# Performance work log

Hardware: AMD Instinct MI355X
Metric: run time of the kernel (lower is better)

## Reference

```python
import jax, jax.numpy as jnp
import numpy as np

D = 1024
H = 16
HD = D // H  # 64


def setup_inputs() -> dict:
    key = jax.random.key(0)
    ks = jax.random.split(key, 11)
    B, L = 2, 2048
    std = 0.02
    return {
        "query": jax.random.normal(ks[0], (B, L, D), jnp.float32),
        "key": jax.random.normal(ks[1], (B, L, D), jnp.float32),
        "value": jax.random.normal(ks[2], (B, L, D), jnp.float32),
        "Wq": jax.random.normal(ks[3], (D, D), jnp.float32) * std,
        "bq": jnp.zeros((D,), jnp.float32),
        "Wk": jax.random.normal(ks[4], (D, D), jnp.float32) * std,
        "bk": jnp.zeros((D,), jnp.float32),
        "Wv": jax.random.normal(ks[5], (D, D), jnp.float32) * std,
        "bv": jnp.zeros((D,), jnp.float32),
        "Wo": jax.random.normal(ks[6], (D, D), jnp.float32) * std,
        "bo": jnp.zeros((D,), jnp.float32),
    }


def _split_heads(x):
    # [B, L, D] -> [B, H, L, HD]
    B, L, _ = x.shape
    return x.reshape(B, L, H, HD).transpose(0, 2, 1, 3)


def reference(query, key, value, Wq, bq, Wk, bk, Wv, bv, Wo, bo):
    B, Lq, _ = query.shape
    # Linear projections (torch Linear: x @ W.T + b)
    Q = _split_heads(query @ Wq.T + bq)
    K = _split_heads(key @ Wk.T + bk)
    V = _split_heads(value @ Wv.T + bv)
    scale = HD ** -0.5
    scores = jnp.einsum("bhqd,bhkd->bhqk", Q, K) * scale  # [B,H,Lq,Lk]
    weights = jax.nn.softmax(scores, axis=-1)
    attended = jnp.einsum("bhqk,bhkd->bhqd", weights, V)  # [B,H,Lq,HD]
    attended = attended.transpose(0, 2, 1, 3).reshape(B, Lq, D)
    output = attended @ Wo.T + bo
    return output, weights.mean(axis=1)
```

## Files before the change

### kernel.cpp

```cpp
#include <hip/hip_runtime.h>
#include <stdint.h>

#define D_MODEL 1024
#define NHEAD 16
#define HDIM 64
#define SEQ 2048
#define NTOK 4096
#define KVB 128
#define NT (KVB / 16)

typedef unsigned short u16;
typedef float f32x4 __attribute__((ext_vector_type(4)));
typedef __bf16 bf16x8 __attribute__((ext_vector_type(8)));
typedef unsigned int u32x4 __attribute__((ext_vector_type(4)));
typedef u16 u16x4 __attribute__((ext_vector_type(4)));

#define QSC 0.180336880111117f

__device__ __forceinline__ u16 fcast_bf(float f) {
  __bf16 h = (__bf16)f;
  return __builtin_bit_cast(u16, h);
}

__device__ __forceinline__ float exp2_fast(float x) {
#if __has_builtin(__builtin_amdgcn_exp2f)
  return __builtin_amdgcn_exp2f(x);
#else
  return __expf(x * 0.69314718056f);
#endif
}

__device__ __forceinline__ bf16x8 scale_q(bf16x8 q) {
  bf16x8 r;
#pragma unroll
  for (int i = 0; i < 8; i++) r[i] = (__bf16)((float)q[i] * QSC);
  return r;
}

__device__ __forceinline__ bf16x8 lds_frag(const u16* sm, int off) {
  return *reinterpret_cast<const bf16x8*>(sm + off);
}

__device__ __forceinline__ void gload_lds16(const u16* g, u16* l) {
  __builtin_amdgcn_global_load_lds((const __attribute__((address_space(1))) void*)g,
                                   (__attribute__((address_space(3))) void*)l, 16, 0, 0);
}

__global__ void cvt3_kernel(const float* __restrict__ s0, const float* __restrict__ s1,
                            const float* __restrict__ s2, u16* __restrict__ dst, int n4) {
  const float* s = blockIdx.y == 0 ? s0 : (blockIdx.y == 1 ? s1 : s2);
  u16* d = dst + (size_t)blockIdx.y * n4 * 4;
  int i = blockIdx.x * blockDim.x + threadIdx.x;
  int stride = gridDim.x * blockDim.x;
  for (; i < n4; i += stride) {
    f32x4 v = reinterpret_cast<const f32x4*>(s)[i];
    u16x4 o;
    o[0] = fcast_bf(v[0]); o[1] = fcast_bf(v[1]);
    o[2] = fcast_bf(v[2]); o[3] = fcast_bf(v[3]);
    reinterpret_cast<u16x4*>(d)[i] = o;
  }
}

__global__ void cvt4_kernel(const float* __restrict__ s0, const float* __restrict__ s1,
                            const float* __restrict__ s2, const float* __restrict__ s3,
                            u16* __restrict__ dst, int n4) {
  const float* s = blockIdx.y == 0 ? s0 : (blockIdx.y == 1 ? s1 : (blockIdx.y == 2 ? s2 : s3));
  u16* d = dst + (size_t)blockIdx.y * n4 * 4;
  int i = blockIdx.x * blockDim.x + threadIdx.x;
  int stride = gridDim.x * blockDim.x;
  for (; i < n4; i += stride) {
    f32x4 v = reinterpret_cast<const f32x4*>(s)[i];
    u16x4 o;
    o[0] = fcast_bf(v[0]); o[1] = fcast_bf(v[1]);
    o[2] = fcast_bf(v[2]); o[3] = fcast_bf(v[3]);
    reinterpret_cast<u16x4*>(d)[i] = o;
  }
}

template<int MODE>
__global__ __launch_bounds__(256)
void gemm_kernel(const u16* __restrict__ Abase, const u16* __restrict__ Wbase,
                 const float* __restrict__ b0, const float* __restrict__ b1,
                 const float* __restrict__ b2,
                 u16* __restrict__ obf, float* __restrict__ of32) {
  const int z = (MODE == 0) ? blockIdx.z : 0;
  const u16* A = Abase + (size_t)z * NTOK * D_MODEL;
  const u16* W = Wbase + (size_t)z * D_MODEL * D_MODEL;
  const float* bias = (MODE == 0) ? (z == 0 ? b0 : (z == 1 ? b1 : b2)) : b0;
  u16* oz = (MODE == 0) ? (obf + (size_t)z * NTOK * D_MODEL) : obf;

  const int flat = blockIdx.y * 8 + blockIdx.x;
  const int nf = (flat & 7) * 32 + (flat >> 3);
  const int bn0 = (nf & 7) * 128;
  const int bm0 = (nf >> 3) * 128;
  const int tid = threadIdx.x;
  const int lane = tid & 63, wid = tid >> 6;
  const int wm = wid >> 1, wn = wid & 1;
  const int l15 = lane & 15, l4 = lane >> 4;
  const int lrow8 = lane >> 3, lch = lane & 7;

  __shared__ u16 smA[128 * 64];
  __shared__ u16 smB[128 * 64];

  f32x4 acc[4][4];
#pragma unroll
  for (int mi = 0; mi < 4; mi++)
#pragma unroll
    for (int ni = 0; ni < 4; ni++) acc[mi][ni] = f32x4{0.f, 0.f, 0.f, 0.f};

  for (int it = 0; it < D_MODEL / 64; it++) {
    const int k0 = it * 64;
    __syncthreads();
#pragma unroll
    for (int c2 = 0; c2 < 4; c2++) {
      int blk = wid * 4 + c2;
      int base16 = blk * 512;
      int row = blk * 8 + lrow8;
      gload_lds16(A + (size_t)(bm0 + row) * D_MODEL + k0 + lch * 8, &smA[base16]);
      gload_lds16(W + (size_t)(bn0 + row) * D_MODEL + k0 + lch * 8, &smB[base16]);
    }
    __syncthreads();
#pragma unroll
    for (int kk = 0; kk < 2; kk++) {
      bf16x8 af[4], bfv[4];
#pragma unroll
      for (int mi = 0; mi < 4; mi++) {
        int r = wm * 64 + mi * 16 + l15;
        af[mi] = lds_frag(smA, r * 64 + (kk * 4 + l4) * 8);
      }
#pragma unroll
      for (int ni = 0; ni < 4; ni++) {
        int r = wn * 64 + ni * 16 + l15;
        bfv[ni] = lds_frag(smB, r * 64 + (kk * 4 + l4) * 8);
      }
#pragma unroll
      for (int mi = 0; mi < 4; mi++)
#pragma unroll
        for (int ni = 0; ni < 4; ni++)
          acc[mi][ni] = __builtin_amdgcn_mfma_f32_16x16x32_bf16(af[mi], bfv[ni], acc[mi][ni], 0, 0, 0);
    }
  }

#pragma unroll
  for (int mi = 0; mi < 4; mi++) {
#pragma unroll
    for (int ni = 0; ni < 4; ni++) {
      int colg = bn0 + wn * 64 + ni * 16 + l15;
      float bv = bias[colg];
      if (MODE == 0 && z == 2) {
        int h = colg >> 6, hd = colg & 63;
        int row0 = bm0 + wm * 64 + mi * 16 + l4 * 4;
        int b = row0 >> 11, lq = row0 & 2047;
        u16x4 pk;
#pragma unroll
        for (int j = 0; j < 4; j++) pk[j] = fcast_bf(acc[mi][ni][j] + bv);
        size_t idx = ((size_t)((b * NHEAD + h) * HDIM + hd)) * SEQ + lq;
        *reinterpret_cast<u16x4*>(oz + idx) = pk;
      } else {
#pragma unroll
        for (int j = 0; j < 4; j++) {
          int rowg = bm0 + wm * 64 + mi * 16 + l4 * 4 + j;
          float v = acc[mi][ni][j] + bv;
          if (MODE == 0) {
            int b = rowg >> 11, lq = rowg & 2047;
            int h = colg >> 6, hd = colg & 63;
            oz[((size_t)((b * NHEAD + h) * SEQ + lq)) * HDIM + hd] = fcast_bf(v);
          } else {
            of32[(size_t)rowg * D_MODEL + colg] = v;
          }
        }
      }
    }
  }
}

__global__ __launch_bounds__(512)
void attn_kernel(const u16* __restrict__ Qh, const u16* __restrict__ Kh,
                 const u16* __restrict__ Vh, u16* __restrict__ attb,
                 float* __restrict__ m_ws, float* __restrict__ linv_ws) {
  const int qt0 = blockIdx.x * 128;
  const int bh = blockIdx.y;
  const int b = bh >> 4, h = bh & 15;
  const int tid = threadIdx.x;
  const int lane = tid & 63, wid = tid >> 6;
  const int l15 = lane & 15, l4 = lane >> 4;

  const u16* Qp = Qh + (size_t)bh * SEQ * HDIM;
  const u16* Kp = Kh + (size_t)bh * SEQ * HDIM;
  const u16* Vp = Vh + (size_t)bh * HDIM * SEQ;

  __shared__ u16 smK[KVB * 64];
  __shared__ u16 smV[64 * KVB];
  __shared__ u16 smP[8][16 * KVB];

  bf16x8 qf[2];
  {
    const u16* qrow = Qp + (size_t)(qt0 + wid * 16 + l15) * HDIM;
    qf[0] = scale_q(*reinterpret_cast<const bf16x8*>(qrow + l4 * 8));
    qf[1] = scale_q(*reinterpret_cast<const bf16x8*>(qrow + 32 + l4 * 8));
  }

  float m = -1e30f, lsum = 0.f;
  f32x4 oacc[4];
#pragma unroll
  for (int d = 0; d < 4; d++) oacc[d] = f32x4{0.f, 0.f, 0.f, 0.f};

  u32x4 rk[2], rv[2];
#pragma unroll
  for (int i = 0; i < 2; i++) {
    int c = i * 512 + tid;
    rk[i] = *reinterpret_cast<const u32x4*>(Kp + (size_t)(c >> 3) * HDIM + (c & 7) * 8);
    rv[i] = *reinterpret_cast<const u32x4*>(Vp + (size_t)(c >> 4) * SEQ + (c & 15) * 8);
  }

  for (int kt = 0; kt < SEQ / KVB; kt++) {
    __syncthreads();
#pragma unroll
    for (int i = 0; i < 2; i++) {
      int c = i * 512 + tid;
      { int row = c >> 3, ch = c & 7;
        *reinterpret_cast<u32x4*>(&smK[row * 64 + ((ch ^ (row & 7)) * 8)]) = rk[i]; }
      { int row = c >> 4, ch = c & 15;
        *reinterpret_cast<u32x4*>(&smV[row * KVB + ((ch ^ (row & 15)) * 8)]) = rv[i]; }
    }
    __syncthreads();
    if (kt + 1 < SEQ / KVB) {
      int kn = (kt + 1) * KVB;
#pragma unroll
      for (int i = 0; i < 2; i++) {
        int c = i * 512 + tid;
        rk[i] = *reinterpret_cast<const u32x4*>(Kp + (size_t)(kn + (c >> 3)) * HDIM + (c & 7) * 8);
        rv[i] = *reinterpret_cast<const u32x4*>(Vp + (size_t)(c >> 4) * SEQ + kn + (c & 15) * 8);
      }
    }
    f32x4 s[NT];
#pragma unroll
    for (int nt = 0; nt < NT; nt++) s[nt] = f32x4{0.f, 0.f, 0.f, 0.f};
#pragma unroll
    for (int kk = 0; kk < 2; kk++) {
#pragma unroll
      for (int nt = 0; nt < NT; nt++) {
        int r = nt * 16 + l15;
        int ch = (kk * 4 + l4) ^ (r & 7);
        bf16x8 kf = lds_frag(smK, r * 64 + ch * 8);
        s[nt] = __builtin_amdgcn_mfma_f32_16x16x32_bf16(kf, qf[kk], s[nt], 0, 0, 0);
      }
    }
    float smax = s[0][0];
#pragma unroll
    for (int nt = 0; nt < NT; nt++)
#pragma unroll
      for (int j = 0; j < 4; j++) smax = fmaxf(smax, s[nt][j]);
    smax = fmaxf(smax, __shfl_xor(smax, 16));
    smax = fmaxf(smax, __shfl_xor(smax, 32));
    float mn = fmaxf(m, smax);
    float corr = exp2_fast(m - mn);
    m = mn;
    float ps = 0.f;
#pragma unroll
    for (int nt = 0; nt < NT; nt++) {
      u16x4 pwv;
#pragma unroll
      for (int j = 0; j < 4; j++) {
        float pv = exp2_fast(s[nt][j] - mn);
        ps += pv;
        pwv[j] = fcast_bf(pv);
      }
      int sp = (nt * 4 + l4) ^ (l15 * 2);
      *reinterpret_cast<u16x4*>(&smP[wid][l15 * KVB + sp * 4]) = pwv;
    }
    ps += __shfl_xor(ps, 16);
    ps += __shfl_xor(ps, 32);
    lsum = lsum * corr + ps;
#pragma unroll
    for (int d = 0; d < 4; d++)
#pragma unroll
      for (int j = 0; j < 4; j++) oacc[d][j] *= corr;
#pragma unroll
    for (int kc = 0; kc < 4; kc++) {
      int chp = (kc * 4 + l4) ^ l15;
      bf16x8 pf = lds_frag(smP[wid], l15 * KVB + chp * 8);
#pragma unroll
      for (int d = 0; d < 4; d++) {
        int r = d * 16 + l15;
        int ch = (kc * 4 + l4) ^ (r & 15);
        bf16x8 vf = lds_frag(smV, r * KVB + ch * 8);
        oacc[d] = __builtin_amdgcn_mfma_f32_16x16x32_bf16(vf, pf, oacc[d], 0, 0, 0);
      }
    }
  }

  const float li = 1.f / lsum;
  const int token = qt0 + wid * 16 + l15;
  if (l4 == 0) {
    m_ws[(size_t)bh * SEQ + token] = m;
    linv_ws[(size_t)bh * SEQ + token] = li;
  }
#pragma unroll
  for (int d = 0; d < 4; d++) {
    u16x4 pk;
#pragma unroll
    for (int j = 0; j < 4; j++) pk[j] = fcast_bf(oacc[d][j] * li);
    *reinterpret_cast<u16x4*>(
        attb + ((size_t)(b * SEQ + token)) * D_MODEL + h * HDIM + d * 16 + l4 * 4) = pk;
  }
}

__global__ __launch_bounds__(512)
void mean_kernel(const u16* __restrict__ Qh, const u16* __restrict__ Kh,
                 const float* __restrict__ m_ws, const float* __restrict__ linv_ws,
                 float* __restrict__ out1) {
  const int kt0 = blockIdx.x * 128;
  const int qt0 = blockIdx.y * 128;
  const int b = blockIdx.z;
  const int tid = threadIdx.x;
  const int lane = tid & 63, wid = tid >> 6;
  const int l15 = lane & 15, l4 = lane >> 4;

  __shared__ u16 smK[2][2][64 * 64];

  f32x4 macc[2][4];
#pragma unroll
  for (int t = 0; t < 2; t++)
#pragma unroll
    for (int nt = 0; nt < 4; nt++) macc[t][nt] = f32x4{0.f, 0.f, 0.f, 0.f};

  const int rbase = qt0 + wid * 16 + l4 * 4;
  const size_t qoff = (size_t)(qt0 + wid * 16 + l15) * HDIM;
  const int srow = tid >> 3, sch = tid & 7;
  const int soff = srow * 64 + ((sch ^ (srow & 7)) * 8);

  u32x4 rk[2];
  bf16x8 qfa, qfb;
  {
    const u16* Kp0 = Kh + (size_t)(b * NHEAD) * SEQ * HDIM;
#pragma unroll
    for (int t = 0; t < 2; t++)
      rk[t] = *reinterpret_cast<const u32x4*>(Kp0 + (size_t)(kt0 + t * 64 + srow) * HDIM + sch * 8);
    const u16* Qp0 = Qh + (size_t)(b * NHEAD) * SEQ * HDIM + qoff;
    qfa = scale_q(*reinterpret_cast<const bf16x8*>(Qp0 + l4 * 8));
    qfb = scale_q(*reinterpret_cast<const bf16x8*>(Qp0 + 32 + l4 * 8));
  }

  for (int h = 0; h < NHEAD; h++) {
    const int bh = b * NHEAD + h;
#pragma unroll
    for (int t = 0; t < 2; t++)
      *reinterpret_cast<u32x4*>(&smK[h & 1][t][soff]) = rk[t];
    __syncthreads();
    u32x4 rkn[2];
    bf16x8 qfan, qfbn;
    if (h + 1 < NHEAD) {
      const u16* Kp1 = Kh + (size_t)(bh + 1) * SEQ * HDIM;
#pragma unroll
      for (int t = 0; t < 2; t++)
        rkn[t] = *reinterpret_cast<const u32x4*>(Kp1 + (size_t)(kt0 + t * 64 + srow) * HDIM + sch * 8);
      const u16* Qp1 = Qh + (size_t)(bh + 1) * SEQ * HDIM + qoff;
      qfan = scale_q(*reinterpret_cast<const bf16x8*>(Qp1 + l4 * 8));
      qfbn = scale_q(*reinterpret_cast<const bf16x8*>(Qp1 + 32 + l4 * 8));
    }
    f32x4 mv = *reinterpret_cast<const f32x4*>(&m_ws[(size_t)bh * SEQ + rbase]);
    f32x4 lv = *reinterpret_cast<const f32x4*>(&linv_ws[(size_t)bh * SEQ + rbase]);
#pragma unroll
    for (int t = 0; t < 2; t++) {
      const u16* kbuf = &smK[h & 1][t][0];
      f32x4 s[4];
#pragma unroll
      for (int nt = 0; nt < 4; nt++) s[nt] = f32x4{0.f, 0.f, 0.f, 0.f};
#pragma unroll
      for (int kk = 0; kk < 2; kk++) {
#pragma unroll
        for (int nt = 0; nt < 4; nt++) {
          int r = nt * 16 + l15;
          int ch = (kk * 4 + l4) ^ (r & 7);
          bf16x8 kf = lds_frag(kbuf, r * 64 + ch * 8);
          s[nt] = __builtin_amdgcn_mfma_f32_16x16x32_bf16(kk == 0 ? qfa : qfb, kf, s[nt], 0, 0, 0);
        }
      }
#pragma unroll
      for (int nt = 0; nt < 4; nt++)
#pragma unroll
        for (int j = 0; j < 4; j++)
          macc[t][nt][j] += exp2_fast(s[nt][j] - mv[j]) * lv[j];
    }
    if (h + 1 < NHEAD) {
      rk[0] = rkn[0]; rk[1] = rkn[1];
      qfa = qfan; qfb = qfbn;
    }
  }
  const float invh = 1.f / 16.f;
#pragma unroll
  for (int t = 0; t < 2; t++)
#pragma unroll
    for (int nt = 0; nt < 4; nt++)
#pragma unroll
      for (int j = 0; j < 4; j++)
        out1[((size_t)(b * SEQ + rbase + j)) * SEQ + kt0 + t * 64 + nt * 16 + l15] =
            macc[t][nt][j] * invh;
}

extern "C" void kernel_launch(void* const* d_in, const int* in_sizes, int n_in,
                              void* d_out, int out_size, void* d_ws, size_t ws_size,
                              hipStream_t stream) {
  (void)in_sizes; (void)n_in; (void)out_size; (void)ws_size;
  const float* query = (const float*)d_in[0];
  const float* key = (const float*)d_in[1];
  const float* value = (const float*)d_in[2];
  const float* Wq = (const float*)d_in[3];
  const float* bq = (const float*)d_in[4];
  const float* Wk = (const float*)d_in[5];
  const float* bk = (const float*)d_in[6];
  const float* Wv = (const float*)d_in[7];
  const float* bv = (const float*)d_in[8];
  const float* Wo = (const float*)d_in[9];
  const float* bo = (const float*)d_in[10];

  char* ws = (char*)d_ws;
  u16* xb = (u16*)(ws);
  u16* wb = (u16*)(ws + 25165824);
  u16* Qhp = (u16*)(ws + 33554432);
  u16* attb = (u16*)(ws + 58720256);
  float* m_ws = (float*)(ws + 67108864);
  float* linv_ws = (float*)(ws + 67371008);

  float* out0 = (float*)d_out;
  float* out1 = out0 + (size_t)NTOK * D_MODEL;

  cvt3_kernel<<<dim3(512, 3), 256, 0, stream>>>(query, key, value, xb, 1048576);
  cvt4_kernel<<<dim3(192, 4), 256, 0, stream>>>(Wq, Wk, Wv, Wo, wb, 262144);

  gemm_kernel<0><<<dim3(8, 32, 3), 256, 0, stream>>>(xb, wb, bq, bk, bv, Qhp, nullptr);
  attn_kernel<<<dim3(16, 32), 512, 0, stream>>>(Qhp, Qhp + 4194304, Qhp + 8388608,
                                                attb, m_ws, linv_ws);
  mean_kernel<<<dim3(16, 16, 2), 512, 0, stream>>>(Qhp, Qhp + 4194304, m_ws, linv_ws, out1);
  gemm_kernel<1><<<dim3(8, 32, 1), 256, 0, stream>>>(attb, wb + 3 * 1048576, bo, bo, bo,
                                                     nullptr, out0);
}
```

Measured before the change: 190.3 us.

## Merge conversion launches and co-schedule weight-mean with output projection

The two fp32-to-bf16 conversion kernels become one launch over seven sources. The separate mean-weights kernel and output-projection GEMM become one 768-block 'tail' launch, with blocks split by index between the two jobs. This removes launch gaps and lets the bandwidth-bound mean work overlap the MFMA-bound projection. The projection part uses 512 threads with a 2x4 per-wave tile, so each wave computes half as many outputs and has less reuse per LDS load than the old 256-thread kernel.

```diff
diff --git a/kernel.cpp b/kernel.cpp
--- a/kernel.cpp
+++ b/kernel.cpp
@@ -46,48 +46,36 @@
                                    (__attribute__((address_space(3))) void*)l, 16, 0, 0);
 }
 
-__global__ void cvt3_kernel(const float* __restrict__ s0, const float* __restrict__ s1,
-                            const float* __restrict__ s2, u16* __restrict__ dst, int n4) {
-  const float* s = blockIdx.y == 0 ? s0 : (blockIdx.y == 1 ? s1 : s2);
-  u16* d = dst + (size_t)blockIdx.y * n4 * 4;
+__global__ void cvt_all_kernel(const float* __restrict__ q, const float* __restrict__ k,
+                               const float* __restrict__ v, const float* __restrict__ wq,
+                               const float* __restrict__ wk, const float* __restrict__ wv,
+                               const float* __restrict__ wo, u16* __restrict__ dst) {
+  const int y = blockIdx.y;
+  const float* s = y == 0 ? q : (y == 1 ? k : (y == 2 ? v : (y == 3 ? wq :
+                   (y == 4 ? wk : (y == 5 ? wv : wo)))));
+  const int n4 = y < 3 ? 1048576 : 262144;
+  const size_t off4 = y < 3 ? (size_t)y * 1048576 : 3145728 + (size_t)(y - 3) * 262144;
+  u16x4* d = reinterpret_cast<u16x4*>(dst) + off4;
   int i = blockIdx.x * blockDim.x + threadIdx.x;
   int stride = gridDim.x * blockDim.x;
   for (; i < n4; i += stride) {
-    f32x4 v = reinterpret_cast<const f32x4*>(s)[i];
+    f32x4 vv = reinterpret_cast<const f32x4*>(s)[i];
     u16x4 o;
-    o[0] = fcast_bf(v[0]); o[1] = fcast_bf(v[1]);
-    o[2] = fcast_bf(v[2]); o[3] = fcast_bf(v[3]);
-    reinterpret_cast<u16x4*>(d)[i] = o;
-  }
-}
-
-__global__ void cvt4_kernel(const float* __restrict__ s0, const float* __restrict__ s1,
-                            const float* __restrict__ s2, const float* __restrict__ s3,
-                            u16* __restrict__ dst, int n4) {
-  const float* s = blockIdx.y == 0 ? s0 : (blockIdx.y == 1 ? s1 : (blockIdx.y == 2 ? s2 : s3));
-  u16* d = dst + (size_t)blockIdx.y * n4 * 4;
-  int i = blockIdx.x * blockDim.x + threadIdx.x;
-  int stride = gridDim.x * blockDim.x;
-  for (; i < n4; i += stride) {
-    f32x4 v = reinterpret_cast<const f32x4*>(s)[i];
-    u16x4 o;
-    o[0] = fcast_bf(v[0]); o[1] = fcast_bf(v[1]);
-    o[2] = fcast_bf(v[2]); o[3] = fcast_bf(v[3]);
-    reinterpret_cast<u16x4*>(d)[i] = o;
-  }
-}
-
-template<int MODE>
+    o[0] = fcast_bf(vv[0]); o[1] = fcast_bf(vv[1]);
+    o[2] = fcast_bf(vv[2]); o[3] = fcast_bf(vv[3]);
+    d[i] = o;
+  }
+}
+
 __global__ __launch_bounds__(256)
-void gemm_kernel(const u16* __restrict__ Abase, const u16* __restrict__ Wbase,
-                 const float* __restrict__ b0, const float* __restrict__ b1,
-                 const float* __restrict__ b2,
-                 u16* __restrict__ obf, float* __restrict__ of32) {
-  const int z = (MODE == 0) ? blockIdx.z : 0;
+void gemm_qkv_kernel(const u16* __restrict__ Abase, const u16* __restrict__ Wbase,
+                     const float* __restrict__ b0, const float* __restrict__ b1,
+                     const float* __restrict__ b2, u16* __restrict__ obf) {
+  const int z = blockIdx.z;
   const u16* A = Abase + (size_t)z * NTOK * D_MODEL;
   const u16* W = Wbase + (size_t)z * D_MODEL * D_MODEL;
-  const float* bias = (MODE == 0) ? (z == 0 ? b0 : (z == 1 ? b1 : b2)) : b0;
-  u16* oz = (MODE == 0) ? (obf + (size_t)z * NTOK * D_MODEL) : obf;
+  const float* bias = z == 0 ? b0 : (z == 1 ? b1 : b2);
+  u16* oz = obf + (size_t)z * NTOK * D_MODEL;
 
   const int flat = blockIdx.y * 8 + blockIdx.x;
   const int nf = (flat & 7) * 32 + (flat >> 3);
@@ -147,7 +135,7 @@
     for (int ni = 0; ni < 4; ni++) {
       int colg = bn0 + wn * 64 + ni * 16 + l15;
       float bv = bias[colg];
-      if (MODE == 0 && z == 2) {
+      if (z == 2) {
         int h = colg >> 6, hd = colg & 63;
         int row0 = bm0 + wm * 64 + mi * 16 + l4 * 4;
         int b = row0 >> 11, lq = row0 & 2047;
@@ -161,13 +149,9 @@
         for (int j = 0; j < 4; j++) {
           int rowg = bm0 + wm * 64 + mi * 16 + l4 * 4 + j;
           float v = acc[mi][ni][j] + bv;
-          if (MODE == 0) {
-            int b = rowg >> 11, lq = rowg & 2047;
-            int h = colg >> 6, hd = colg & 63;
-            oz[((size_t)((b * NHEAD + h) * SEQ + lq)) * HDIM + hd] = fcast_bf(v);
-          } else {
-            of32[(size_t)rowg * D_MODEL + colg] = v;
-          }
+          int b = rowg >> 11, lq = rowg & 2047;
+          int h = colg >> 6, hd = colg & 63;
+          oz[((size_t)((b * NHEAD + h) * SEQ + lq)) * HDIM + hd] = fcast_bf(v);
         }
       }
     }
@@ -307,96 +291,163 @@
 }
 
 __global__ __launch_bounds__(512)
-void mean_kernel(const u16* __restrict__ Qh, const u16* __restrict__ Kh,
+void tail_kernel(const u16* __restrict__ Qh, const u16* __restrict__ Kh,
                  const float* __restrict__ m_ws, const float* __restrict__ linv_ws,
-                 float* __restrict__ out1) {
-  const int kt0 = blockIdx.x * 128;
-  const int qt0 = blockIdx.y * 128;
-  const int b = blockIdx.z;
+                 float* __restrict__ out1,
+                 const u16* __restrict__ attb, const u16* __restrict__ Wo,
+                 const float* __restrict__ bo, float* __restrict__ out0) {
+  __shared__ u16 smem[16384];
+  const int bid = blockIdx.x;
   const int tid = threadIdx.x;
   const int lane = tid & 63, wid = tid >> 6;
   const int l15 = lane & 15, l4 = lane >> 4;
 
-  __shared__ u16 smK[2][2][64 * 64];
-
-  f32x4 macc[2][4];
-#pragma unroll
-  for (int t = 0; t < 2; t++)
-#pragma unroll
-    for (int nt = 0; nt < 4; nt++) macc[t][nt] = f32x4{0.f, 0.f, 0.f, 0.f};
-
-  const int rbase = qt0 + wid * 16 + l4 * 4;
-  const size_t qoff = (size_t)(qt0 + wid * 16 + l15) * HDIM;
-  const int srow = tid >> 3, sch = tid & 7;
-  const int soff = srow * 64 + ((sch ^ (srow & 7)) * 8);
-
-  u32x4 rk[2];
-  bf16x8 qfa, qfb;
-  {
-    const u16* Kp0 = Kh + (size_t)(b * NHEAD) * SEQ * HDIM;
+  if (bid < 512) {
+    const int kt0 = (bid & 15) * 128;
+    const int qt0 = ((bid >> 4) & 15) * 128;
+    const int b = bid >> 8;
+
+    f32x4 macc[2][4];
 #pragma unroll
     for (int t = 0; t < 2; t++)
-      rk[t] = *reinterpret_cast<const u32x4*>(Kp0 + (size_t)(kt0 + t * 64 + srow) * HDIM + sch * 8);
-    const u16* Qp0 = Qh + (size_t)(b * NHEAD) * SEQ * HDIM + qoff;
-    qfa = scale_q(*reinterpret_cast<const bf16x8*>(Qp0 + l4 * 8));
-    qfb = scale_q(*reinterpret_cast<const bf16x8*>(Qp0 + 32 + l4 * 8));
-  }
-
-  for (int h = 0; h < NHEAD; h++) {
-    const int bh = b * NHEAD + h;
+#pragma unroll
+      for (int nt = 0; nt < 4; nt++) macc[t][nt] = f32x4{0.f, 0.f, 0.f, 0.f};
+
+    const int rbase = qt0 + wid * 16 + l4 * 4;
+    const size_t qoff = (size_t)(qt0 + wid * 16 + l15) * HDIM;
+    const int srow = tid >> 3, sch = tid & 7;
+    const int soff = srow * 64 + ((sch ^ (srow & 7)) * 8);
+
+    u32x4 rk[2];
+    bf16x8 qfa, qfb;
+    {
+      const u16* Kp0 = Kh + (size_t)(b * NHEAD) * SEQ * HDIM;
+#pragma unroll
+      for (int t = 0; t < 2; t++)
+        rk[t] = *reinterpret_cast<const u32x4*>(Kp0 + (size_t)(kt0 + t * 64 + srow) * HDIM + sch * 8);
+      const u16* Qp0 = Qh + (size_t)(b * NHEAD) * SEQ * HDIM + qoff;
+      qfa = scale_q(*reinterpret_cast<const bf16x8*>(Qp0 + l4 * 8));
+      qfb = scale_q(*reinterpret_cast<const bf16x8*>(Qp0 + 32 + l4 * 8));
+    }
+
+    for (int h = 0; h < NHEAD; h++) {
+      const int bh = b * NHEAD + h;
+#pragma unroll
+      for (int t = 0; t < 2; t++)
+        *reinterpret_cast<u32x4*>(&smem[((h & 1) * 2 + t) * 4096 + soff]) = rk[t];
+      __syncthreads();
+      u32x4 rkn[2];
+      bf16x8 qfan, qfbn;
+      if (h + 1 < NHEAD) {
+        const u16* Kp1 = Kh + (size_t)(bh + 1) * SEQ * HDIM;
+#pragma unroll
+        for (int t = 0; t < 2; t++)
+          rkn[t] = *reinterpret_cast<const u32x4*>(Kp1 + (size_t)(kt0 + t * 64 + srow) * HDIM + sch * 8);
+        const u16* Qp1 = Qh + (size_t)(bh + 1) * SEQ * HDIM + qoff;
+        qfan = scale_q(*reinterpret_cast<const bf16x8*>(Qp1 + l4 * 8));
+        qfbn = scale_q(*reinterpret_cast<const bf16x8*>(Qp1 + 32 + l4 * 8));
+      }
+      f32x4 mv = *reinterpret_cast<const f32x4*>(&m_ws[(size_t)bh * SEQ + rbase]);
+      f32x4 lv = *reinterpret_cast<const f32x4*>(&linv_ws[(size_t)bh * SEQ + rbase]);
+#pragma unroll
+      for (int t = 0; t < 2; t++) {
+        const u16* kbuf = &smem[((h & 1) * 2 + t) * 4096];
+        f32x4 s[4];
+#pragma unroll
+        for (int nt = 0; nt < 4; nt++) s[nt] = f32x4{0.f, 0.f, 0.f, 0.f};
+#pragma unroll
+        for (int kk = 0; kk < 2; kk++) {
+#pragma unroll
+          for (int nt = 0; nt < 4; nt++) {
+            int r = nt * 16 + l15;
+            int ch = (kk * 4 + l4) ^ (r & 7);
+            bf16x8 kf = lds_frag(kbuf, r * 64 + ch * 8);
+            s[nt] = __builtin_amdgcn_mfma_f32_16x16x32_bf16(kk == 0 ? qfa : qfb, kf, s[nt], 0, 0, 0);
+          }
+        }
+#pragma unroll
+        for (int nt = 0; nt < 4; nt++)
+#pragma unroll
+          for (int j = 0; j < 4; j++)
+            macc[t][nt][j] += exp2_fast(s[nt][j] - mv[j]) * lv[j];
+      }
+      if (h + 1 < NHEAD) {
+        rk[0] = rkn[0]; rk[1] = rkn[1];
+        qfa = qfan; qfb = qfbn;
+      }
+    }
+    const float invh = 1.f / 16.f;
 #pragma unroll
     for (int t = 0; t < 2; t++)
-      *reinterpret_cast<u32x4*>(&smK[h & 1][t][soff]) = rk[t];
-    __syncthreads();
-    u32x4 rkn[2];
-    bf16x8 qfan, qfbn;
-    if (h + 1 < NHEAD) {
-      const u16* Kp1 = Kh + (size_t)(bh + 1) * SEQ * HDIM;
-#pragma unroll
-      for (int t = 0; t < 2; t++)
-        rkn[t] = *reinterpret_cast<const u32x4*>(Kp1 + (size_t)(kt0 + t * 64 + srow) * HDIM + sch * 8);
-      const u16* Qp1 = Qh + (size_t)(bh + 1) * SEQ * HDIM + qoff;
-      qfan = scale_q(*reinterpret_cast<const bf16x8*>(Qp1 + l4 * 8));
-      qfbn = scale_q(*reinterpret_cast<const bf16x8*>(Qp1 + 32 + l4 * 8));
-    }
-    f32x4 mv = *reinterpret_cast<const f32x4*>(&m_ws[(size_t)bh * SEQ + rbase]);
-    f32x4 lv = *reinterpret_cast<const f32x4*>(&linv_ws[(size_t)bh * SEQ + rbase]);
-#pragma unroll
-    for (int t = 0; t < 2; t++) {
-      const u16* kbuf = &smK[h & 1][t][0];
-      f32x4 s[4];
-#pragma unroll
-      for (int nt = 0; nt < 4; nt++) s[nt] = f32x4{0.f, 0.f, 0.f, 0.f};
+#pragma unroll
+      for (int nt = 0; nt < 4; nt++)
+#pragma unroll
+        for (int j = 0; j < 4; j++)
+          out1[((size_t)(b * SEQ + rbase + j)) * SEQ + kt0 + t * 64 + nt * 16 + l15] =
+              macc[t][nt][j] * invh;
+  } else {
+    const int flat = bid - 512;
+    const int nf = (flat & 7) * 32 + (flat >> 3);
+    const int bn0 = (nf & 7) * 128;
+    const int bm0 = (nf >> 3) * 128;
+    const int wm = wid >> 1, wn = wid & 1;
+    const int lrow8 = lane >> 3, lch = lane & 7;
+    u16* smA = smem;
+    u16* smB = smem + 8192;
+
+    f32x4 acc[2][4];
+#pragma unroll
+    for (int mi = 0; mi < 2; mi++)
+#pragma unroll
+      for (int ni = 0; ni < 4; ni++) acc[mi][ni] = f32x4{0.f, 0.f, 0.f, 0.f};
+
+    for (int it = 0; it < D_MODEL / 64; it++) {
+      const int k0 = it * 64;
+      __syncthreads();
+#pragma unroll
+      for (int c2 = 0; c2 < 2; c2++) {
+        int blk = wid * 2 + c2;
+        int base16 = blk * 512;
+        int row = blk * 8 + lrow8;
+        gload_lds16(attb + (size_t)(bm0 + row) * D_MODEL + k0 + lch * 8, &smA[base16]);
+        gload_lds16(Wo + (size_t)(bn0 + row) * D_MODEL + k0 + lch * 8, &smB[base16]);
+      }
+      __syncthreads();
 #pragma unroll
       for (int kk = 0; kk < 2; kk++) {
-#pragma unroll
-        for (int nt = 0; nt < 4; nt++) {
-          int r = nt * 16 + l15;
-          int ch = (kk * 4 + l4) ^ (r & 7);
-          bf16x8 kf = lds_frag(kbuf, r * 64 + ch * 8);
-          s[nt] = __builtin_amdgcn_mfma_f32_16x16x32_bf16(kk == 0 ? qfa : qfb, kf, s[nt], 0, 0, 0);
+        bf16x8 af[2], bfv[4];
+#pragma unroll
+        for (int mi = 0; mi < 2; mi++) {
+          int r = wm * 32 + mi * 16 + l15;
+          af[mi] = lds_frag(smA, r * 64 + (kk * 4 + l4) * 8);
         }
-      }
-#pragma unroll
-      for (int nt = 0; nt < 4; nt++)
-#pragma unroll
-        for (int j = 0; j < 4; j++)
-          macc[t][nt][j] += exp2_fast(s[nt][j] - mv[j]) * lv[j];
-    }
-    if (h + 1 < NHEAD) {
-      rk[0] = rkn[0]; rk[1] = rkn[1];
-      qfa = qfan; qfb = qfbn;
-    }
-  }
-  const float invh = 1.f / 16.f;
-#pragma unroll
-  for (int t = 0; t < 2; t++)
-#pragma unroll
-    for (int nt = 0; nt < 4; nt++)
-#pragma unroll
-      for (int j = 0; j < 4; j++)
-        out1[((size_t)(b * SEQ + rbase + j)) * SEQ + kt0 + t * 64 + nt * 16 + l15] =
-            macc[t][nt][j] * invh;
+#pragma unroll
+        for (int ni = 0; ni < 4; ni++) {
+          int r = wn * 64 + ni * 16 + l15;
+          bfv[ni] = lds_frag(smB, r * 64 + (kk * 4 + l4) * 8);
+        }
+#pragma unroll
+        for (int mi = 0; mi < 2; mi++)
+#pragma unroll
+          for (int ni = 0; ni < 4; ni++)
+            acc[mi][ni] = __builtin_amdgcn_mfma_f32_16x16x32_bf16(af[mi], bfv[ni], acc[mi][ni], 0, 0, 0);
+      }
+    }
+
+#pragma unroll
+    for (int mi = 0; mi < 2; mi++) {
+#pragma unroll
+      for (int ni = 0; ni < 4; ni++) {
+        int colg = bn0 + wn * 64 + ni * 16 + l15;
+        float bv = bo[colg];
+#pragma unroll
+        for (int j = 0; j < 4; j++) {
+          int rowg = bm0 + wm * 32 + mi * 16 + l4 * 4 + j;
+          out0[(size_t)rowg * D_MODEL + colg] = acc[mi][ni][j] + bv;
+        }
+      }
+    }
+  }
 }
 
 extern "C" void kernel_launch(void* const* d_in, const int* in_sizes, int n_in,
@@ -426,13 +477,11 @@
   float* out0 = (float*)d_out;
   float* out1 = out0 + (size_t)NTOK * D_MODEL;
 
-  cvt3_kernel<<<dim3(512, 3), 256, 0, stream>>>(query, key, value, xb, 1048576);
-  cvt4_kernel<<<dim3(192, 4), 256, 0, stream>>>(Wq, Wk, Wv, Wo, wb, 262144);
-
-  gemm_kernel<0><<<dim3(8, 32, 3), 256, 0, stream>>>(xb, wb, bq, bk, bv, Qhp, nullptr);
+  cvt_all_kernel<<<dim3(256, 7), 256, 0, stream>>>(query, key, value, Wq, Wk, Wv, Wo, xb);
+
+  gemm_qkv_kernel<<<dim3(8, 32, 3), 256, 0, stream>>>(xb, wb, bq, bk, bv, Qhp);
   attn_kernel<<<dim3(16, 32), 512, 0, stream>>>(Qhp, Qhp + 4194304, Qhp + 8388608,
                                                 attb, m_ws, linv_ws);
-  mean_kernel<<<dim3(16, 16, 2), 512, 0, stream>>>(Qhp, Qhp + 4194304, m_ws, linv_ws, out1);
-  gemm_kernel<1><<<dim3(8, 32, 1), 256, 0, stream>>>(attb, wb + 3 * 1048576, bo, bo, bo,
-                                                     nullptr, out0);
-}
+  tail_kernel<<<768, 512, 0, stream>>>(Qhp, Qhp + 4194304, m_ws, linv_ws, out1,
+                                       attb, wb + 3 * 1048576, bo, out0);
+}
```

Result: faster. 185.8 us (-2.3%).
